# Optimization experiments

Hardware: AMD Instinct MI355X
Metric: run time of the kernel (lower is better)

The kernel has to match this reference:

```python
import jax, jax.numpy as jnp
import numpy as np

EMB = 64
HID = 1024
SEQ = 9
BATCH = 4096


def setup_inputs() -> dict:
    key = jax.random.key(0)
    ks = jax.random.split(key, 10)
    s = lambda *sh: 1.0 / np.sqrt(sh[-1])
    return {
        "observed": jax.random.normal(ks[0], (SEQ, BATCH, 2), dtype=jnp.float32),
        "W_emb": jax.random.normal(ks[1], (EMB, 2), dtype=jnp.float32) * s(2),
        "b_emb": jnp.zeros((EMB,), dtype=jnp.float32),
        "W_ih": jax.random.normal(ks[2], (4 * HID, EMB), dtype=jnp.float32) * s(EMB),
        "b_ih": jnp.zeros((4 * HID,), dtype=jnp.float32),
        "W_hh": jax.random.normal(ks[3], (4 * HID, HID), dtype=jnp.float32) * s(HID),
        "b_hh": jnp.zeros((4 * HID,), dtype=jnp.float32),
        "W_out": jax.random.normal(ks[4], (5, HID), dtype=jnp.float32) * s(HID),
        "b_out": jnp.zeros((5,), dtype=jnp.float32),
        "n_predict": 12,
    }


def _cell(x, h, c, W_ih, b_ih, W_hh, b_hh):
    # torch.nn.LSTMCell gate math, gate order i, f, g, o
    gates = x @ W_ih.T + b_ih + h @ W_hh.T + b_hh  # [B, 4H]
    i, f, g, o = jnp.split(gates, 4, axis=-1)
    c_new = jax.nn.sigmoid(f) * c + jax.nn.sigmoid(i) * jnp.tanh(g)
    h_new = jax.nn.sigmoid(o) * jnp.tanh(c_new)
    return h_new, c_new


def reference(observed, W_emb, b_emb, W_ih, b_ih, W_hh, b_hh, W_out, b_out, n_predict):
    B = observed.shape[1]
    H = W_hh.shape[1]
    h0 = jnp.zeros((B, H), dtype=observed.dtype)
    c0 = jnp.zeros((B, H), dtype=observed.dtype)

    diffs = observed[1:] - observed[:-1]  # [SEQ-1, B, 2]

    def obs_step(carry, d):
        h, c = carry
        emb = jax.nn.relu(d @ W_emb.T + b_emb)  # [B, EMB]
        h, c = _cell(emb, h, c, W_ih, b_ih, W_hh, b_hh)
        normal = h @ W_out.T + b_out  # [B, 5]
        return (h, c), normal

    (h, c), normals_obs = jax.lax.scan(obs_step, (h0, c0), diffs)
    new_vel = normals_obs[-1][:, :2]

    def pred_step(carry, _):
        h, c, nv = carry
        emb = jax.nn.relu(jax.lax.stop_gradient(nv) @ W_emb.T + b_emb)
        h, c = _cell(emb, h, c, W_ih, b_ih, W_hh, b_hh)
        normal = h @ W_out.T + b_out
        return (h, c, normal[:, :2]), normal

    (_, _, _), normals_pred = jax.lax.scan(
        pred_step, (h, c, new_vel), None, length=n_predict - 1)

    # training-mode output: stacked raw 'normal' params, shape [SEQ-1+n_predict-1, B, 5]
    return jnp.concatenate([normals_obs, normals_pred], axis=0)
```

## Files before the change

kernel.cpp:

```cpp
#include <hip/hip_runtime.h>
#include <stdint.h>
#include <stddef.h>

#define BATCH 4096
#define HID   1024
#define EMB   64
#define NKH   32
#define NSTEP 19
#define NOBS  8
#define WSL   139264

typedef _Float16 f16;
typedef _Float16 half8 __attribute__((ext_vector_type(8)));
typedef float    float4v __attribute__((ext_vector_type(4)));

__device__ __forceinline__ float sigm(float x) { return 1.f / (1.f + __expf(-x)); }
__device__ __forceinline__ float tanh_f(float x) { return 1.f - 2.f / (__expf(2.f * x) + 1.f); }

__global__ void pack_kernel(const float* __restrict__ W_ih, const float* __restrict__ b_ih,
                            const float* __restrict__ W_hh, const float* __restrict__ b_hh,
                            f16* __restrict__ Wsw, float* __restrict__ bc) {
  int gid = blockIdx.x * blockDim.x + threadIdx.x;
  int tt = gid / WSL;
  int rem = gid - tt * WSL;
  int kt = rem >> 12;
  int ni = (rem >> 9) & 7;
  int lane = (rem >> 3) & 63;
  int e = rem & 7;
  int p = tt * 128 + ni * 16 + (lane & 15);
  int g = (p >> 5) & 3;
  int u = p & 31;
  int orig = g * HID + tt * 32 + u;
  int k = kt * 32 + ((lane >> 4) << 3) + e;
  float val = (k < EMB) ? W_ih[orig * EMB + k] : W_hh[orig * HID + (k - EMB)];
  Wsw[gid] = (f16)val;
  if (k == 0) bc[p] = b_ih[orig] + b_hh[orig];
}

__global__ __launch_bounds__(256, 2)
void gemm_cell_kernel(const f16* __restrict__ Xp, const f16* __restrict__ Wsw,
                      const float* __restrict__ bc,
                      f16* __restrict__ c_ws, f16* __restrict__ Xn,
                      float* __restrict__ po_ws, const float* __restrict__ W_out,
                      const float* __restrict__ obs_t, const float* __restrict__ outprev,
                      int mode, const float* __restrict__ W_emb,
                      const float* __restrict__ b_emb) {
  const int tid = threadIdx.x;
  const int lane = tid & 63;
  const int w = tid >> 6;
  const int l15 = lane & 15;
  const int quad = lane >> 4;
  const int id = blockIdx.x;
  const int x = id & 7, s = id >> 3;
  const int tt = ((x >> 1) << 3) | (s & 7);
  const int mB = ((x & 1) << 3) | (s >> 3);
  const int rt0 = mB * 16 + w * 4;

  const f16* aB = Xp + (size_t)rt0 * (NKH * 512) + lane * 8;
  const f16* bB = Wsw + (size_t)tt * WSL + lane * 8;

  float4v acc[4][8];
#pragma unroll
  for (int mi = 0; mi < 4; ++mi)
#pragma unroll
    for (int ni = 0; ni < 8; ++ni) acc[mi][ni] = (float4v){0.f, 0.f, 0.f, 0.f};

  {
    float d0[4], d1[4];
#pragma unroll
    for (int mi = 0; mi < 4; ++mi) {
      const int row = (rt0 + mi) * 16 + l15;
      if (mode <= 1) {
        const float* o = obs_t + row * 2;
        d0[mi] = o[BATCH * 2] - o[0];
        d1[mi] = o[BATCH * 2 + 1] - o[1];
      } else {
        d0[mi] = outprev[(size_t)row * 5 + 0];
        d1[mi] = outprev[(size_t)row * 5 + 1];
      }
    }
#pragma unroll
    for (int kt = 0; kt < 2; ++kt) {
      float w0[8], w1[8], be[8];
#pragma unroll
      for (int e = 0; e < 8; ++e) {
        int j = kt * 32 + quad * 8 + e;
        w0[e] = W_emb[2 * j];
        w1[e] = W_emb[2 * j + 1];
        be[e] = b_emb[j];
      }
      half8 bf[8];
#pragma unroll
      for (int ni = 0; ni < 8; ++ni) bf[ni] = *(const half8*)(bB + kt * 4096 + ni * 512);
#pragma unroll
      for (int mi = 0; mi < 4; ++mi) {
        half8 ae;
#pragma unroll
        for (int e = 0; e < 8; ++e)
          ae[e] = (f16)fmaxf(d0[mi] * w0[e] + d1[mi] * w1[e] + be[e], 0.f);
#pragma unroll
        for (int ni = 0; ni < 8; ++ni)
          acc[mi][ni] = __builtin_amdgcn_mfma_f32_16x16x32_f16(ae, bf[ni], acc[mi][ni], 0, 0, 0);
      }
    }
  }

  if (mode >= 1) {
    half8 afA[4], bfA[8], afB[4], bfB[8];
#define LOADF(af, bf, kh)                                                          \
  do {                                                                             \
    _Pragma("unroll") for (int mi = 0; mi < 4; ++mi)                               \
        af[mi] = *(const half8*)(aB + mi * (NKH * 512) + (kh) * 512);              \
    _Pragma("unroll") for (int ni = 0; ni < 8; ++ni)                               \
        bf[ni] = *(const half8*)(bB + ((kh) + 2) * 4096 + ni * 512);               \
  } while (0)
#define MFMA_ALL(af, bf)                                                           \
  do {                                                                             \
    _Pragma("unroll") for (int mi = 0; mi < 4; ++mi)                               \
    _Pragma("unroll") for (int ni = 0; ni < 8; ++ni)                               \
        acc[mi][ni] =                                                              \
            __builtin_amdgcn_mfma_f32_16x16x32_f16(af[mi], bf[ni], acc[mi][ni], 0, 0, 0); \
  } while (0)
    LOADF(afA, bfA, 0);
    for (int i = 0; i < NKH / 2; ++i) {
      const int k1 = 2 * i + 1;
      LOADF(afB, bfB, k1);
      MFMA_ALL(afA, bfA);
      if (k1 + 1 < NKH) LOADF(afA, bfA, k1 + 1);
      MFMA_ALL(afB, bfB);
    }
#undef LOADF
#undef MFMA_ALL
  }

  float bias[8];
#pragma unroll
  for (int ni = 0; ni < 8; ++ni) bias[ni] = bc[tt * 128 + ni * 16 + l15];
  float wb[2][5];
#pragma unroll
  for (int u16 = 0; u16 < 2; ++u16)
#pragma unroll
    for (int o = 0; o < 5; ++o)
      wb[u16][o] = W_out[o * HID + tt * 32 + u16 * 16 + l15];

  f16* cbase = c_ws + ((size_t)(mB * 32 + tt) * 256 + tid) * 32;
  half8 cv8[4];
#pragma unroll
  for (int q = 0; q < 4; ++q) cv8[q] = *(const half8*)(cbase + q * 8);

#pragma unroll
  for (int mi = 0; mi < 4; ++mi) {
#pragma unroll
    for (int r = 0; r < 4; ++r) {
      const int row = mB * 256 + w * 64 + mi * 16 + quad * 4 + r;
      float pa[5] = {0.f, 0.f, 0.f, 0.f, 0.f};
#pragma unroll
      for (int u16 = 0; u16 < 2; ++u16) {
        const int ce = (mi * 2 + u16) * 4 + r;
        float gi = acc[mi][u16 + 0][r] + bias[u16 + 0];
        float gf = acc[mi][u16 + 2][r] + bias[u16 + 2];
        float gg = acc[mi][u16 + 4][r] + bias[u16 + 4];
        float go = acc[mi][u16 + 6][r] + bias[u16 + 6];
        float co = (mode == 0) ? 0.f : (float)cv8[ce >> 3][ce & 7];
        float cn = sigm(gf) * co + sigm(gi) * tanh_f(gg);
        cv8[ce >> 3][ce & 7] = (f16)cn;
        float h = sigm(go) * tanh_f(cn);
        Xn[(((size_t)(row >> 4) * NKH + tt) * 64 + (row & 15) + 16 * (u16 * 2 + (l15 >> 3))) * 8 +
           (l15 & 7)] = (f16)h;
#pragma unroll
        for (int o = 0; o < 5; ++o) pa[o] += h * wb[u16][o];
      }
#pragma unroll
      for (int o = 0; o < 5; ++o) {
        pa[o] += __shfl_xor(pa[o], 1, 64);
        pa[o] += __shfl_xor(pa[o], 2, 64);
        pa[o] += __shfl_xor(pa[o], 4, 64);
        pa[o] += __shfl_xor(pa[o], 8, 64);
      }
      if (l15 == 0) {
        float* pdst = po_ws + ((size_t)tt * BATCH + row) * 5;
#pragma unroll
        for (int o = 0; o < 5; ++o) pdst[o] = pa[o];
      }
    }
  }
#pragma unroll
  for (int q = 0; q < 4; ++q) *(half8*)(cbase + q * 8) = cv8[q];
}

__global__ __launch_bounds__(256)
void reduce_kernel(const float* __restrict__ po_ws, const float* __restrict__ b_out,
                   float* __restrict__ out_t) {
  const int tid = threadIdx.x;
  const int r0 = blockIdx.x * 32;
  if (tid < 160) {
    const int rowl = tid / 5, o = tid - rowl * 5;
    const int row = r0 + rowl;
    float s = 0.f;
#pragma unroll
    for (int tt = 0; tt < 32; ++tt) s += po_ws[((size_t)tt * BATCH + row) * 5 + o];
    out_t[(size_t)row * 5 + o] = s + b_out[o];
  }
}

extern "C" void kernel_launch(void* const* d_in, const int* in_sizes, int n_in,
                              void* d_out, int out_size, void* d_ws, size_t ws_size,
                              hipStream_t stream) {
  const float* observed = (const float*)d_in[0];
  const float* W_emb = (const float*)d_in[1];
  const float* b_emb = (const float*)d_in[2];
  const float* W_ih = (const float*)d_in[3];
  const float* b_ih = (const float*)d_in[4];
  const float* W_hh = (const float*)d_in[5];
  const float* b_hh = (const float*)d_in[6];
  const float* W_out = (const float*)d_in[7];
  const float* b_out = (const float*)d_in[8];
  float* out = (float*)d_out;

  uint8_t* ws = (uint8_t*)d_ws;
  const size_t WSW_BYTES = (size_t)32 * WSL * sizeof(f16);
  const size_t XH_BYTES = (size_t)256 * NKH * 64 * 8 * sizeof(f16);
  f16* Wsw = (f16*)ws;
  float* bc = (float*)(ws + WSW_BYTES);
  f16* X0 = (f16*)(ws + WSW_BYTES + 16384);
  f16* X1 = (f16*)(ws + WSW_BYTES + 16384 + XH_BYTES);
  f16* c_ws = (f16*)(ws + WSW_BYTES + 16384 + 2 * XH_BYTES);
  float* po_ws = (float*)(ws + WSW_BYTES + 16384 + 2 * XH_BYTES + (size_t)BATCH * HID * 2);

  pack_kernel<<<(32 * WSL) / 256, 256, 0, stream>>>(W_ih, b_ih, W_hh, b_hh, Wsw, bc);

  for (int t = 0; t < NSTEP; ++t) {
    f16* Xc = (t & 1) ? X1 : X0;
    f16* Xp = (t & 1) ? X0 : X1;
    const int mode = (t == 0) ? 0 : (t < NOBS ? 1 : 2);
    gemm_cell_kernel<<<512, 256, 0, stream>>>(
        Xp, Wsw, bc, c_ws, Xc, po_ws, W_out,
        observed + (size_t)t * BATCH * 2, out + (size_t)(t - 1) * BATCH * 5,
        mode, W_emb, b_emb);
    reduce_kernel<<<BATCH / 32, 256, 0, stream>>>(po_ws, b_out, out + (size_t)t * BATCH * 5);
  }
}
```

Measured before the change: 1.065 ms.

## Stage LSTM GEMM tiles through LDS and fuse output projection via atomics

Restructures the per-step gate GEMM into 256 blocks of 512 threads. Each block stages its A (hidden state) and B (weight) tiles into double-buffered LDS with global_load_lds, so waves in a block share the loaded operands instead of each loading its own. The weight packing is reordered so every wave owns all four gates for 16 hidden units. The separate reduce kernel is removed: each wave atomically adds its partial output-projection sums into the output, which is pre-filled with b_out by a new init kernel. This cuts launches and workspace traffic, at the cost of atomic contention and a non-deterministic summation order.

Measured after the change: 3.617 ms. 240% more time.

```diff
diff --git a/kernel.cpp b/kernel.cpp
--- a/kernel.cpp
+++ b/kernel.cpp
@@ -16,6 +16,13 @@
 
 __device__ __forceinline__ float sigm(float x) { return 1.f / (1.f + __expf(-x)); }
 __device__ __forceinline__ float tanh_f(float x) { return 1.f - 2.f / (__expf(2.f * x) + 1.f); }
+
+typedef const __attribute__((address_space(1))) unsigned int gau32;
+typedef __attribute__((address_space(3))) unsigned int lau32;
+
+__device__ __forceinline__ void gload16(const void* src, void* lds) {
+  __builtin_amdgcn_global_load_lds((gau32*)src, (lau32*)lds, 16, 0, 0);
+}
 
 __global__ void pack_kernel(const float* __restrict__ W_ih, const float* __restrict__ b_ih,
                             const float* __restrict__ W_hh, const float* __restrict__ b_hh,
@@ -28,50 +35,81 @@
   int lane = (rem >> 3) & 63;
   int e = rem & 7;
   int p = tt * 128 + ni * 16 + (lane & 15);
-  int g = (p >> 5) & 3;
-  int u = p & 31;
-  int orig = g * HID + tt * 32 + u;
+  int g = (p >> 4) & 3;
+  int u = (p >> 8) * 64 + ((p >> 6) & 3) * 16 + (p & 15);
+  int orig = g * HID + u;
   int k = kt * 32 + ((lane >> 4) << 3) + e;
   float val = (k < EMB) ? W_ih[orig * EMB + k] : W_hh[orig * HID + (k - EMB)];
   Wsw[gid] = (f16)val;
   if (k == 0) bc[p] = b_ih[orig] + b_hh[orig];
 }
 
-__global__ __launch_bounds__(256, 2)
+__global__ __launch_bounds__(1024)
+void init_out_kernel(const float* __restrict__ b_out, float* __restrict__ out) {
+  int i = blockIdx.x * 1024 + threadIdx.x;
+  out[i] = b_out[i % 5];
+}
+
+__global__ __launch_bounds__(512, 2)
 void gemm_cell_kernel(const f16* __restrict__ Xp, const f16* __restrict__ Wsw,
                       const float* __restrict__ bc,
                       f16* __restrict__ c_ws, f16* __restrict__ Xn,
-                      float* __restrict__ po_ws, const float* __restrict__ W_out,
+                      float* __restrict__ out_t, const float* __restrict__ W_out,
                       const float* __restrict__ obs_t, const float* __restrict__ outprev,
                       int mode, const float* __restrict__ W_emb,
                       const float* __restrict__ b_emb) {
+  __shared__ f16 smem[65536];
+
   const int tid = threadIdx.x;
   const int lane = tid & 63;
   const int w = tid >> 6;
   const int l15 = lane & 15;
   const int quad = lane >> 4;
+  const int wm = w >> 2, wn = w & 3;
+  const int sh = wn >> 1, nq = wn & 1;
+
   const int id = blockIdx.x;
-  const int x = id & 7, s = id >> 3;
-  const int tt = ((x >> 1) << 3) | (s & 7);
-  const int mB = ((x & 1) << 3) | (s >> 3);
-  const int rt0 = mB * 16 + w * 4;
-
-  const f16* aB = Xp + (size_t)rt0 * (NKH * 512) + lane * 8;
-  const f16* bB = Wsw + (size_t)tt * WSL + lane * 8;
-
-  float4v acc[4][8];
-#pragma unroll
-  for (int mi = 0; mi < 4; ++mi)
-#pragma unroll
-    for (int ni = 0; ni < 8; ++ni) acc[mi][ni] = (float4v){0.f, 0.f, 0.f, 0.f};
+  const int x = id & 7, rr0 = id >> 3;
+  const int bn = x * 2 + (rr0 & 1);
+  const int bm = rr0 >> 1;
+  const int slice = bn * 2 + sh;
+
+  float4v acc[8][4];
+#pragma unroll
+  for (int mi = 0; mi < 8; ++mi)
+#pragma unroll
+    for (int ni = 0; ni < 4; ++ni) acc[mi][ni] = (float4v){0.f, 0.f, 0.f, 0.f};
+
+  auto stage = [&](int sp) {
+    const int p2 = sp & 1;
+    const int khg = 2 * (sp - 1);
+#pragma unroll
+    for (int i = 0; i < 4; ++i) {
+      const int c = wn * 4 + i;
+      const int rtl = wm * 8 + (c >> 1), khl = c & 1;
+      const f16* src = Xp + ((size_t)(bm * 16 + rtl) * NKH + (khg + khl)) * 512 + lane * 8;
+      f16* dst = smem + p2 * 32768 + (rtl * 2 + khl) * 512;
+      gload16(src, dst);
+    }
+#pragma unroll
+    for (int i = 0; i < 4; ++i) {
+      const int c = (wm * 2 + nq) * 4 + i;
+      const int nisl = c >> 1, khl = c & 1;
+      const f16* src = Wsw + (size_t)slice * WSL + (2 + khg + khl) * 4096 + nisl * 512 + lane * 8;
+      f16* dst = smem + p2 * 32768 + 16384 + ((sh * 8 + nisl) * 2 + khl) * 512;
+      gload16(src, dst);
+    }
+  };
+
+  if (mode != 0) stage(1);
 
   {
-    float d0[4], d1[4];
-#pragma unroll
-    for (int mi = 0; mi < 4; ++mi) {
-      const int row = (rt0 + mi) * 16 + l15;
+    float d0[8], d1[8];
+#pragma unroll
+    for (int mi = 0; mi < 8; ++mi) {
+      const int row = (bm * 16 + wm * 8 + mi) * 16 + l15;
       if (mode <= 1) {
-        const float* o = obs_t + row * 2;
+        const float* o = obs_t + (size_t)row * 2;
         d0[mi] = o[BATCH * 2] - o[0];
         d1[mi] = o[BATCH * 2 + 1] - o[1];
       } else {
@@ -84,92 +122,100 @@
       float w0[8], w1[8], be[8];
 #pragma unroll
       for (int e = 0; e < 8; ++e) {
-        int j = kt * 32 + quad * 8 + e;
+        const int j = kt * 32 + quad * 8 + e;
         w0[e] = W_emb[2 * j];
         w1[e] = W_emb[2 * j + 1];
         be[e] = b_emb[j];
       }
-      half8 bf[8];
-#pragma unroll
-      for (int ni = 0; ni < 8; ++ni) bf[ni] = *(const half8*)(bB + kt * 4096 + ni * 512);
-#pragma unroll
-      for (int mi = 0; mi < 4; ++mi) {
+      half8 bfe[4];
+#pragma unroll
+      for (int ni = 0; ni < 4; ++ni)
+        bfe[ni] = *(const half8*)(Wsw + (size_t)slice * WSL + kt * 4096 + (nq * 4 + ni) * 512 + lane * 8);
+#pragma unroll
+      for (int mi = 0; mi < 8; ++mi) {
         half8 ae;
 #pragma unroll
         for (int e = 0; e < 8; ++e)
           ae[e] = (f16)fmaxf(d0[mi] * w0[e] + d1[mi] * w1[e] + be[e], 0.f);
 #pragma unroll
-        for (int ni = 0; ni < 8; ++ni)
-          acc[mi][ni] = __builtin_amdgcn_mfma_f32_16x16x32_f16(ae, bf[ni], acc[mi][ni], 0, 0, 0);
-      }
-    }
-  }
-
-  if (mode >= 1) {
-    half8 afA[4], bfA[8], afB[4], bfB[8];
-#define LOADF(af, bf, kh)                                                          \
-  do {                                                                             \
-    _Pragma("unroll") for (int mi = 0; mi < 4; ++mi)                               \
-        af[mi] = *(const half8*)(aB + mi * (NKH * 512) + (kh) * 512);              \
-    _Pragma("unroll") for (int ni = 0; ni < 8; ++ni)                               \
-        bf[ni] = *(const half8*)(bB + ((kh) + 2) * 4096 + ni * 512);               \
-  } while (0)
-#define MFMA_ALL(af, bf)                                                           \
-  do {                                                                             \
-    _Pragma("unroll") for (int mi = 0; mi < 4; ++mi)                               \
-    _Pragma("unroll") for (int ni = 0; ni < 8; ++ni)                               \
-        acc[mi][ni] =                                                              \
-            __builtin_amdgcn_mfma_f32_16x16x32_f16(af[mi], bf[ni], acc[mi][ni], 0, 0, 0); \
-  } while (0)
-    LOADF(afA, bfA, 0);
-    for (int i = 0; i < NKH / 2; ++i) {
-      const int k1 = 2 * i + 1;
-      LOADF(afB, bfB, k1);
-      MFMA_ALL(afA, bfA);
-      if (k1 + 1 < NKH) LOADF(afA, bfA, k1 + 1);
-      MFMA_ALL(afB, bfB);
-    }
-#undef LOADF
-#undef MFMA_ALL
-  }
-
-  float bias[8];
-#pragma unroll
-  for (int ni = 0; ni < 8; ++ni) bias[ni] = bc[tt * 128 + ni * 16 + l15];
-  float wb[2][5];
-#pragma unroll
-  for (int u16 = 0; u16 < 2; ++u16)
-#pragma unroll
-    for (int o = 0; o < 5; ++o)
-      wb[u16][o] = W_out[o * HID + tt * 32 + u16 * 16 + l15];
-
-  f16* cbase = c_ws + ((size_t)(mB * 32 + tt) * 256 + tid) * 32;
-  half8 cv8[4];
-#pragma unroll
-  for (int q = 0; q < 4; ++q) cv8[q] = *(const half8*)(cbase + q * 8);
-
-#pragma unroll
-  for (int mi = 0; mi < 4; ++mi) {
+        for (int ni = 0; ni < 4; ++ni)
+          acc[mi][ni] = __builtin_amdgcn_mfma_f32_16x16x32_f16(ae, bfe[ni], acc[mi][ni], 0, 0, 0);
+      }
+    }
+  }
+
+  if (mode != 0) {
+    for (int s = 1; s <= 16; ++s) {
+      __syncthreads();
+      if (s < 16) stage(s + 1);
+
+      const f16* base = smem + (s & 1) * 32768;
+      half8 a[8][2], b8[4][2];
+#pragma unroll
+      for (int mi = 0; mi < 8; ++mi)
+#pragma unroll
+        for (int khl = 0; khl < 2; ++khl)
+          a[mi][khl] = *(const half8*)(base + ((wm * 8 + mi) * 2 + khl) * 512 + lane * 8);
+#pragma unroll
+      for (int ni = 0; ni < 4; ++ni)
+#pragma unroll
+        for (int khl = 0; khl < 2; ++khl)
+          b8[ni][khl] = *(const half8*)(base + 16384 + ((sh * 8 + nq * 4 + ni) * 2 + khl) * 512 + lane * 8);
+
+#pragma unroll
+      for (int mh = 0; mh < 2; ++mh)
+#pragma unroll
+        for (int nh = 0; nh < 2; ++nh) {
+          __builtin_amdgcn_s_setprio(1);
+#pragma unroll
+          for (int m2 = 0; m2 < 4; ++m2)
+#pragma unroll
+            for (int n2 = 0; n2 < 2; ++n2)
+#pragma unroll
+              for (int khl = 0; khl < 2; ++khl) {
+                const int mi = mh * 4 + m2, ni = nh * 2 + n2;
+                acc[mi][ni] =
+                    __builtin_amdgcn_mfma_f32_16x16x32_f16(a[mi][khl], b8[ni][khl], acc[mi][ni], 0, 0, 0);
+              }
+          __builtin_amdgcn_s_setprio(0);
+        }
+    }
+  }
+
+  float bb[4];
+#pragma unroll
+  for (int ni = 0; ni < 4; ++ni) bb[ni] = bc[bn * 256 + wn * 64 + ni * 16 + l15];
+  const int u = bn * 64 + wn * 16 + l15;
+  float wo[5];
+#pragma unroll
+  for (int o = 0; o < 5; ++o) wo[o] = W_out[o * HID + u];
+
+  f16* cbase = c_ws + (((size_t)(bm * 16 + bn) * 8 + w) * 64 + lane) * 32;
+  half8 cv[4];
+  if (mode != 0) {
+#pragma unroll
+    for (int q = 0; q < 4; ++q) cv[q] = *(const half8*)(cbase + q * 8);
+  }
+
+#pragma unroll
+  for (int mi = 0; mi < 8; ++mi) {
 #pragma unroll
     for (int r = 0; r < 4; ++r) {
-      const int row = mB * 256 + w * 64 + mi * 16 + quad * 4 + r;
-      float pa[5] = {0.f, 0.f, 0.f, 0.f, 0.f};
-#pragma unroll
-      for (int u16 = 0; u16 < 2; ++u16) {
-        const int ce = (mi * 2 + u16) * 4 + r;
-        float gi = acc[mi][u16 + 0][r] + bias[u16 + 0];
-        float gf = acc[mi][u16 + 2][r] + bias[u16 + 2];
-        float gg = acc[mi][u16 + 4][r] + bias[u16 + 4];
-        float go = acc[mi][u16 + 6][r] + bias[u16 + 6];
-        float co = (mode == 0) ? 0.f : (float)cv8[ce >> 3][ce & 7];
-        float cn = sigm(gf) * co + sigm(gi) * tanh_f(gg);
-        cv8[ce >> 3][ce & 7] = (f16)cn;
-        float h = sigm(go) * tanh_f(cn);
-        Xn[(((size_t)(row >> 4) * NKH + tt) * 64 + (row & 15) + 16 * (u16 * 2 + (l15 >> 3))) * 8 +
-           (l15 & 7)] = (f16)h;
-#pragma unroll
-        for (int o = 0; o < 5; ++o) pa[o] += h * wb[u16][o];
-      }
+      const int row = bm * 256 + wm * 128 + mi * 16 + quad * 4 + r;
+      const int ci = mi * 4 + r;
+      float gi = acc[mi][0][r] + bb[0];
+      float gf = acc[mi][1][r] + bb[1];
+      float gg = acc[mi][2][r] + bb[2];
+      float go = acc[mi][3][r] + bb[3];
+      float co = (mode == 0) ? 0.f : (float)cv[ci >> 3][ci & 7];
+      float cn = sigm(gf) * co + sigm(gi) * tanh_f(gg);
+      cv[ci >> 3][ci & 7] = (f16)cn;
+      float h = sigm(go) * tanh_f(cn);
+      Xn[(((size_t)(row >> 4) * NKH + slice) * 64 + (quad * 4 + r) +
+          16 * ((wn & 1) * 2 + (l15 >> 3))) * 8 + (l15 & 7)] = (f16)h;
+      float pa[5];
+#pragma unroll
+      for (int o = 0; o < 5; ++o) pa[o] = h * wo[o];
 #pragma unroll
       for (int o = 0; o < 5; ++o) {
         pa[o] += __shfl_xor(pa[o], 1, 64);
@@ -178,29 +224,13 @@
         pa[o] += __shfl_xor(pa[o], 8, 64);
       }
       if (l15 == 0) {
-        float* pdst = po_ws + ((size_t)tt * BATCH + row) * 5;
-#pragma unroll
-        for (int o = 0; o < 5; ++o) pdst[o] = pa[o];
-      }
-    }
-  }
-#pragma unroll
-  for (int q = 0; q < 4; ++q) *(half8*)(cbase + q * 8) = cv8[q];
-}
-
-__global__ __launch_bounds__(256)
-void reduce_kernel(const float* __restrict__ po_ws, const float* __restrict__ b_out,
-                   float* __restrict__ out_t) {
-  const int tid = threadIdx.x;
-  const int r0 = blockIdx.x * 32;
-  if (tid < 160) {
-    const int rowl = tid / 5, o = tid - rowl * 5;
-    const int row = r0 + rowl;
-    float s = 0.f;
-#pragma unroll
-    for (int tt = 0; tt < 32; ++tt) s += po_ws[((size_t)tt * BATCH + row) * 5 + o];
-    out_t[(size_t)row * 5 + o] = s + b_out[o];
-  }
+#pragma unroll
+        for (int o = 0; o < 5; ++o) atomicAdd(out_t + (size_t)row * 5 + o, pa[o]);
+      }
+    }
+  }
+#pragma unroll
+  for (int q = 0; q < 4; ++q) *(half8*)(cbase + q * 8) = cv[q];
 }
 
 extern "C" void kernel_launch(void* const* d_in, const int* in_sizes, int n_in,
@@ -225,18 +255,17 @@
   f16* X0 = (f16*)(ws + WSW_BYTES + 16384);
   f16* X1 = (f16*)(ws + WSW_BYTES + 16384 + XH_BYTES);
   f16* c_ws = (f16*)(ws + WSW_BYTES + 16384 + 2 * XH_BYTES);
-  float* po_ws = (float*)(ws + WSW_BYTES + 16384 + 2 * XH_BYTES + (size_t)BATCH * HID * 2);
 
   pack_kernel<<<(32 * WSL) / 256, 256, 0, stream>>>(W_ih, b_ih, W_hh, b_hh, Wsw, bc);
+  init_out_kernel<<<(NSTEP * BATCH * 5) / 1024, 1024, 0, stream>>>(b_out, out);
 
   for (int t = 0; t < NSTEP; ++t) {
     f16* Xc = (t & 1) ? X1 : X0;
-    f16* Xp = (t & 1) ? X0 : X1;
+    f16* Xq = (t & 1) ? X0 : X1;
     const int mode = (t == 0) ? 0 : (t < NOBS ? 1 : 2);
-    gemm_cell_kernel<<<512, 256, 0, stream>>>(
-        Xp, Wsw, bc, c_ws, Xc, po_ws, W_out,
+    gemm_cell_kernel<<<256, 512, 0, stream>>>(
+        Xq, Wsw, bc, c_ws, Xc, out + (size_t)t * BATCH * 5, W_out,
         observed + (size_t)t * BATCH * 2, out + (size_t)(t - 1) * BATCH * 5,
         mode, W_emb, b_emb);
-    reduce_kernel<<<BATCH / 32, 256, 0, stream>>>(po_ws, b_out, out + (size_t)t * BATCH * 5);
-  }
-}
+  }
+}
```
